# Kernel tuning notes

Hardware: AMD Instinct MI355X
Metric: run time of the kernel (lower is better)

## Reference

```python
import jax, jax.numpy as jnp
import numpy as np

NTOKENS = 50257
EMB = 1024
N = 8192
K = 10            # noise_ratio
NORM_TERM = 9.0   # lnZ


def setup_inputs() -> dict:
    key = jax.random.key(0)
    k1, k2, k3, k4, k5, k6 = jax.random.split(key, 6)
    inp = jax.random.normal(k1, (N, EMB), dtype=jnp.float32)
    target = jax.random.randint(k2, (N,), 0, NTOKENS)
    noise_samples = jax.random.randint(k3, (N, K), 0, NTOKENS)
    # decoder params (nn.Linear(emb_size, ntokens)): weight (V, E), bias (V)
    bound = 1.0 / np.sqrt(EMB)
    weight = jax.random.uniform(k4, (NTOKENS, EMB), minval=-bound, maxval=bound, dtype=jnp.float32)
    bias = jax.random.uniform(k5, (NTOKENS,), minval=-bound, maxval=bound, dtype=jnp.float32)
    # noise distribution over the vocabulary (normalized)
    p = jax.random.uniform(k6, (NTOKENS,), minval=0.1, maxval=1.0, dtype=jnp.float32)
    noise = p / jnp.sum(p)
    return {"input": inp, "weight": weight, "bias": bias, "noise": noise,
            "target": target, "noise_samples": noise_samples}


def reference(input, weight, bias, noise, target, noise_samples):
    # indices per token: [target, noise_0..noise_{k-1}] -> (N, K+1)
    idx = jnp.concatenate([target[:, None], noise_samples], axis=1)
    w = weight[idx]                      # (N, K+1, E) gathered rows
    b = bias[idx]                        # (N, K+1)
    logits = jnp.einsum('ne,nke->nk', input, w) + b
    probs = jnp.exp(logits - NORM_TERM)  # unnormalized model probs
    data_prob = probs[:, 0]              # (N,)
    noise_in_data_probs = probs[:, 1:]   # (N, K)
    noise_probs = noise[noise_samples]   # (N, K)
    k = jnp.float32(K)
    rnn_loss = jnp.log(data_prob / (data_prob + k * noise[target]))
    noise_loss = jnp.sum(
        jnp.log(k * noise_probs / (noise_in_data_probs + k * noise_probs)), axis=1)
    loss = -jnp.sum(rnn_loss + noise_loss)
    return loss / N  # size_average=True
```

## Files before the change

kernel.cpp:

```cpp
#include <hip/hip_runtime.h>

#define N_TOK 8192
#define EMB 1024
#define KNOISE 10
#define KP1 11
#define NORM_TERM 9.0f

typedef float f4 __attribute__((ext_vector_type(4)));

__global__ __launch_bounds__(256) void nce_token_kernel(
    const float* __restrict__ input,
    const float* __restrict__ weight,
    const float* __restrict__ bias,
    const float* __restrict__ noise,
    const int* __restrict__ target,
    const int* __restrict__ ns,
    float* __restrict__ token_loss)
{
    __shared__ f4 s_in[EMB / 4];
    __shared__ float s_dot[16];

    const int n = blockIdx.x;
    const int tid = threadIdx.x;
    const int wave = tid >> 6;
    const int lane = tid & 63;

    const f4* inrow = reinterpret_cast<const f4*>(input + (size_t)n * EMB);
    s_in[tid] = __builtin_nontemporal_load(&inrow[tid]);
    __syncthreads();

    int rows[3];
    #pragma unroll
    for (int i = 0; i < 3; ++i) {
        const int k = wave + 4 * i;
        rows[i] = (k < KP1) ? ((k == 0) ? target[n] : ns[n * KNOISE + (k - 1)]) : -1;
    }
    const f4* wr[3];
    #pragma unroll
    for (int i = 0; i < 3; ++i)
        wr[i] = reinterpret_cast<const f4*>(weight + (size_t)(rows[i] >= 0 ? rows[i] : 0) * EMB);

    float acc[3] = {0.f, 0.f, 0.f};
    #pragma unroll
    for (int j = 0; j < 4; ++j) {
        const f4 x4 = s_in[lane + 64 * j];
        #pragma unroll
        for (int i = 0; i < 3; ++i) {
            if (rows[i] >= 0) {
                const f4 w4 = wr[i][lane + 64 * j];
                acc[i] = fmaf(w4.x, x4.x, acc[i]);
                acc[i] = fmaf(w4.y, x4.y, acc[i]);
                acc[i] = fmaf(w4.z, x4.z, acc[i]);
                acc[i] = fmaf(w4.w, x4.w, acc[i]);
            }
        }
    }
    #pragma unroll
    for (int off = 32; off > 0; off >>= 1) {
        #pragma unroll
        for (int i = 0; i < 3; ++i)
            acc[i] += __shfl_xor(acc[i], off, 64);
    }
    if (lane == 0) {
        #pragma unroll
        for (int i = 0; i < 3; ++i)
            if (rows[i] >= 0) s_dot[wave + 4 * i] = acc[i] + bias[rows[i]];
    }
    __syncthreads();

    if (tid == 0) {
        const int t = target[n];
        const float p0 = expf(s_dot[0] - NORM_TERM);
        const float kn0 = (float)KNOISE * noise[t];
        float loss = logf(p0 / (p0 + kn0));
        #pragma unroll
        for (int k = 0; k < KNOISE; ++k) {
            const int s = ns[n * KNOISE + k];
            const float pk = expf(s_dot[k + 1] - NORM_TERM);
            const float kn = (float)KNOISE * noise[s];
            loss += logf(kn / (pk + kn));
        }
        __builtin_nontemporal_store(loss, &token_loss[n]);
    }
}

__global__ __launch_bounds__(256) void nce_reduce_kernel(
    const float* __restrict__ token_loss, float* __restrict__ out)
{
    __shared__ float s_part[4];
    float acc = 0.f;
    for (int i = threadIdx.x; i < N_TOK; i += 256)
        acc += __builtin_nontemporal_load(&token_loss[i]);
    #pragma unroll
    for (int off = 32; off > 0; off >>= 1)
        acc += __shfl_xor(acc, off, 64);
    const int wave = threadIdx.x >> 6;
    const int lane = threadIdx.x & 63;
    if (lane == 0) s_part[wave] = acc;
    __syncthreads();
    if (threadIdx.x == 0) {
        const float total = s_part[0] + s_part[1] + s_part[2] + s_part[3];
        out[0] = -total / (float)N_TOK;
    }
}

extern "C" void kernel_launch(void* const* d_in, const int* in_sizes, int n_in,
                              void* d_out, int out_size, void* d_ws, size_t ws_size,
                              hipStream_t stream) {
    const float* input  = (const float*)d_in[0];
    const float* weight = (const float*)d_in[1];
    const float* bias   = (const float*)d_in[2];
    const float* noise  = (const float*)d_in[3];
    const int* target   = (const int*)d_in[4];
    const int* ns       = (const int*)d_in[5];

    float* token_loss = (float*)d_ws;

    nce_token_kernel<<<N_TOK, 256, 0, stream>>>(
        input, weight, bias, noise, target, ns, token_loss);
    nce_reduce_kernel<<<1, 256, 0, stream>>>(token_loss, (float*)d_out);
}
```

Baseline: 82.22 us.

## Fuse per-token loss and final reduction via last-block ticket counter

Merges the reduction kernel into the token kernel using an atomic ticket, so the last finishing block sums all token losses and writes the output. The per-sample exp/log work is also spread across the wave leaders instead of being serialized on thread 0, and the nontemporal input load is replaced with a plain load. This removes one kernel launch and the serial tail in each block, at the cost of a global atomic per block. The ticket counter in the workspace is never reset and relies on modular wraparound of the count, which assumes it starts at zero.

```diff
diff --git a/kernel.cpp b/kernel.cpp
--- a/kernel.cpp
+++ b/kernel.cpp
@@ -8,37 +8,36 @@
 
 typedef float f4 __attribute__((ext_vector_type(4)));
 
-__global__ __launch_bounds__(256) void nce_token_kernel(
+__global__ __launch_bounds__(256) void nce_fused_kernel(
     const float* __restrict__ input,
     const float* __restrict__ weight,
     const float* __restrict__ bias,
     const float* __restrict__ noise,
     const int* __restrict__ target,
     const int* __restrict__ ns,
-    float* __restrict__ token_loss)
+    float* __restrict__ token_loss,
+    unsigned int* __restrict__ ticket,
+    float* __restrict__ out)
 {
     __shared__ f4 s_in[EMB / 4];
-    __shared__ float s_dot[16];
+    __shared__ float s_part[4];
+    __shared__ int s_last;
 
     const int n = blockIdx.x;
     const int tid = threadIdx.x;
     const int wave = tid >> 6;
     const int lane = tid & 63;
 
-    const f4* inrow = reinterpret_cast<const f4*>(input + (size_t)n * EMB);
-    s_in[tid] = __builtin_nontemporal_load(&inrow[tid]);
-    __syncthreads();
+    s_in[tid] = reinterpret_cast<const f4*>(input + (size_t)n * EMB)[tid];
 
     int rows[3];
     #pragma unroll
     for (int i = 0; i < 3; ++i) {
         const int k = wave + 4 * i;
-        rows[i] = (k < KP1) ? ((k == 0) ? target[n] : ns[n * KNOISE + (k - 1)]) : -1;
+        rows[i] = (k == 0) ? target[n]
+                : (k < KP1 ? ns[n * KNOISE + (k - 1)] : -1);
     }
-    const f4* wr[3];
-    #pragma unroll
-    for (int i = 0; i < 3; ++i)
-        wr[i] = reinterpret_cast<const f4*>(weight + (size_t)(rows[i] >= 0 ? rows[i] : 0) * EMB);
+    __syncthreads();
 
     float acc[3] = {0.f, 0.f, 0.f};
     #pragma unroll
@@ -47,7 +46,8 @@
         #pragma unroll
         for (int i = 0; i < 3; ++i) {
             if (rows[i] >= 0) {
-                const f4 w4 = wr[i][lane + 64 * j];
+                const f4 w4 = reinterpret_cast<const f4*>(
+                    weight + (size_t)rows[i] * EMB)[lane + 64 * j];
                 acc[i] = fmaf(w4.x, x4.x, acc[i]);
                 acc[i] = fmaf(w4.y, x4.y, acc[i]);
                 acc[i] = fmaf(w4.z, x4.z, acc[i]);
@@ -61,46 +61,42 @@
         for (int i = 0; i < 3; ++i)
             acc[i] += __shfl_xor(acc[i], off, 64);
     }
+
     if (lane == 0) {
+        float part = 0.f;
         #pragma unroll
-        for (int i = 0; i < 3; ++i)
-            if (rows[i] >= 0) s_dot[wave + 4 * i] = acc[i] + bias[rows[i]];
+        for (int i = 0; i < 3; ++i) {
+            if (rows[i] < 0) continue;
+            const int k = wave + 4 * i;
+            const float logit = acc[i] + bias[rows[i]];
+            const float p = expf(logit - NORM_TERM);
+            const float kn = (float)KNOISE * noise[rows[i]];
+            part += (k == 0) ? logf(p / (p + kn)) : logf(kn / (p + kn));
+        }
+        s_part[wave] = part;
     }
     __syncthreads();
 
     if (tid == 0) {
-        const int t = target[n];
-        const float p0 = expf(s_dot[0] - NORM_TERM);
-        const float kn0 = (float)KNOISE * noise[t];
-        float loss = logf(p0 / (p0 + kn0));
+        token_loss[n] = s_part[0] + s_part[1] + s_part[2] + s_part[3];
+        __threadfence();
+        const unsigned int old = atomicAdd(ticket, 1u);
+        s_last = ((old & (unsigned)(N_TOK - 1)) == (unsigned)(N_TOK - 1)) ? 1 : 0;
+    }
+    __syncthreads();
+
+    if (s_last) {
+        __threadfence();
+        float a = 0.f;
+        for (int i = tid; i < N_TOK; i += 256)
+            a += token_loss[i];
         #pragma unroll
-        for (int k = 0; k < KNOISE; ++k) {
-            const int s = ns[n * KNOISE + k];
-            const float pk = expf(s_dot[k + 1] - NORM_TERM);
-            const float kn = (float)KNOISE * noise[s];
-            loss += logf(kn / (pk + kn));
-        }
-        __builtin_nontemporal_store(loss, &token_loss[n]);
-    }
-}
-
-__global__ __launch_bounds__(256) void nce_reduce_kernel(
-    const float* __restrict__ token_loss, float* __restrict__ out)
-{
-    __shared__ float s_part[4];
-    float acc = 0.f;
-    for (int i = threadIdx.x; i < N_TOK; i += 256)
-        acc += __builtin_nontemporal_load(&token_loss[i]);
-    #pragma unroll
-    for (int off = 32; off > 0; off >>= 1)
-        acc += __shfl_xor(acc, off, 64);
-    const int wave = threadIdx.x >> 6;
-    const int lane = threadIdx.x & 63;
-    if (lane == 0) s_part[wave] = acc;
-    __syncthreads();
-    if (threadIdx.x == 0) {
-        const float total = s_part[0] + s_part[1] + s_part[2] + s_part[3];
-        out[0] = -total / (float)N_TOK;
+        for (int off = 32; off > 0; off >>= 1)
+            a += __shfl_xor(a, off, 64);
+        if (lane == 0) s_part[wave] = a;
+        __syncthreads();
+        if (tid == 0)
+            out[0] = -(s_part[0] + s_part[1] + s_part[2] + s_part[3]) / (float)N_TOK;
     }
 }
 
@@ -114,9 +110,10 @@
     const int* target   = (const int*)d_in[4];
     const int* ns       = (const int*)d_in[5];
 
-    float* token_loss = (float*)d_ws;
+    float* token_loss    = (float*)d_ws;
+    unsigned int* ticket = (unsigned int*)((char*)d_ws + 32768);
 
-    nce_token_kernel<<<N_TOK, 256, 0, stream>>>(
-        input, weight, bias, noise, target, ns, token_loss);
-    nce_reduce_kernel<<<1, 256, 0, stream>>>(token_loss, (float*)d_out);
+    nce_fused_kernel<<<N_TOK, 256, 0, stream>>>(
+        input, weight, bias, noise, target, ns,
+        token_loss, ticket, (float*)d_out);
 }
```

After: 234.4 us. 2.85x slower.

## Split embedding across waves so each thread loads all eleven gathered rows

Applied to the files above, without the earlier changes.

Work is now split by embedding chunk instead of by row. Each thread loads its own slice of the input directly into registers, so the shared-memory staging and its barrier go away, and then issues loads for all 11 gathered weight rows at once. Each wave's partial dot products go to shared memory and are summed across waves, and the loss terms are computed in parallel by 11 lanes instead of one serial thread. This raises memory-level parallelism and removes the idle waves (the old split left one wave with fewer rows), at the cost of more registers and more shuffle work per reduction.

```diff
diff --git a/kernel.cpp b/kernel.cpp
--- a/kernel.cpp
+++ b/kernel.cpp
@@ -17,70 +17,65 @@
     const int* __restrict__ ns,
     float* __restrict__ token_loss)
 {
-    __shared__ f4 s_in[EMB / 4];
-    __shared__ float s_dot[16];
+    __shared__ float s_part[4][12];
 
     const int n = blockIdx.x;
     const int tid = threadIdx.x;
     const int wave = tid >> 6;
     const int lane = tid & 63;
 
-    const f4* inrow = reinterpret_cast<const f4*>(input + (size_t)n * EMB);
-    s_in[tid] = __builtin_nontemporal_load(&inrow[tid]);
-    __syncthreads();
+    int rows[KP1];
+    rows[0] = target[n];
+    #pragma unroll
+    for (int k = 1; k < KP1; ++k)
+        rows[k] = ns[n * KNOISE + k - 1];
 
-    int rows[3];
+    const int off = 64 * wave + lane;
+    const f4 x4 = reinterpret_cast<const f4*>(input + (size_t)n * EMB)[off];
+
+    f4 w[KP1];
     #pragma unroll
-    for (int i = 0; i < 3; ++i) {
-        const int k = wave + 4 * i;
-        rows[i] = (k < KP1) ? ((k == 0) ? target[n] : ns[n * KNOISE + (k - 1)]) : -1;
+    for (int k = 0; k < KP1; ++k)
+        w[k] = reinterpret_cast<const f4*>(weight + (size_t)rows[k] * EMB)[off];
+
+    float acc[KP1];
+    #pragma unroll
+    for (int k = 0; k < KP1; ++k) {
+        float a = w[k].x * x4.x;
+        a = fmaf(w[k].y, x4.y, a);
+        a = fmaf(w[k].z, x4.z, a);
+        a = fmaf(w[k].w, x4.w, a);
+        acc[k] = a;
     }
-    const f4* wr[3];
+
     #pragma unroll
-    for (int i = 0; i < 3; ++i)
-        wr[i] = reinterpret_cast<const f4*>(weight + (size_t)(rows[i] >= 0 ? rows[i] : 0) * EMB);
-
-    float acc[3] = {0.f, 0.f, 0.f};
-    #pragma unroll
-    for (int j = 0; j < 4; ++j) {
-        const f4 x4 = s_in[lane + 64 * j];
+    for (int o = 32; o > 0; o >>= 1) {
         #pragma unroll
-        for (int i = 0; i < 3; ++i) {
-            if (rows[i] >= 0) {
-                const f4 w4 = wr[i][lane + 64 * j];
-                acc[i] = fmaf(w4.x, x4.x, acc[i]);
-                acc[i] = fmaf(w4.y, x4.y, acc[i]);
-                acc[i] = fmaf(w4.z, x4.z, acc[i]);
-                acc[i] = fmaf(w4.w, x4.w, acc[i]);
-            }
-        }
-    }
-    #pragma unroll
-    for (int off = 32; off > 0; off >>= 1) {
-        #pragma unroll
-        for (int i = 0; i < 3; ++i)
-            acc[i] += __shfl_xor(acc[i], off, 64);
+        for (int k = 0; k < KP1; ++k)
+            acc[k] += __shfl_xor(acc[k], o, 64);
     }
     if (lane == 0) {
         #pragma unroll
-        for (int i = 0; i < 3; ++i)
-            if (rows[i] >= 0) s_dot[wave + 4 * i] = acc[i] + bias[rows[i]];
+        for (int k = 0; k < KP1; ++k)
+            s_part[wave][k] = acc[k];
     }
     __syncthreads();
 
-    if (tid == 0) {
-        const int t = target[n];
-        const float p0 = expf(s_dot[0] - NORM_TERM);
-        const float kn0 = (float)KNOISE * noise[t];
-        float loss = logf(p0 / (p0 + kn0));
+    if (wave == 0) {
+        float term = 0.f;
+        if (lane < KP1) {
+            const int row = (lane == 0) ? target[n] : ns[n * KNOISE + lane - 1];
+            const float logit = s_part[0][lane] + s_part[1][lane] +
+                                s_part[2][lane] + s_part[3][lane] + bias[row];
+            const float p = expf(logit - NORM_TERM);
+            const float kn = (float)KNOISE * noise[row];
+            const float num = (lane == 0) ? p : kn;
+            term = logf(num / (p + kn));
+        }
         #pragma unroll
-        for (int k = 0; k < KNOISE; ++k) {
-            const int s = ns[n * KNOISE + k];
-            const float pk = expf(s_dot[k + 1] - NORM_TERM);
-            const float kn = (float)KNOISE * noise[s];
-            loss += logf(kn / (pk + kn));
-        }
-        __builtin_nontemporal_store(loss, &token_loss[n]);
+        for (int o = 8; o > 0; o >>= 1)
+            term += __shfl_xor(term, o, 16);
+        if (lane == 0) token_loss[n] = term;
     }
 }
 
@@ -90,7 +85,7 @@
     __shared__ float s_part[4];
     float acc = 0.f;
     for (int i = threadIdx.x; i < N_TOK; i += 256)
-        acc += __builtin_nontemporal_load(&token_loss[i]);
+        acc += token_loss[i];
     #pragma unroll
     for (int off = 32; off > 0; off >>= 1)
         acc += __shfl_xor(acc, off, 64);
```

Result: faster. 71.56 us (-13.0%).
